# Kernel tuning notes

Measured on AMD Instinct MI355X. Metric: run time of the kernel, lower is better.

Reference implementation:

```python
import jax, jax.numpy as jnp
import numpy as np

B, T, DM, H, DQ, FF, L, OUT = 4, 512, 768, 8, 32, 3072, 6, 80
D_REL = 100   # relative_positional_distance
NEG = 1e8
LN_EPS = 1e-5


def _layer_norm(x, w, b):
    mu = jnp.mean(x, axis=-1, keepdims=True)
    var = jnp.mean((x - mu) ** 2, axis=-1, keepdims=True)
    return (x - mu) * jax.lax.rsqrt(var + LN_EPS) * w + b


def _attention(x, wq, wk, wv, wo, rel):
    # x: (B,T,DM); wq/wk/wv: (H,DM,DQ); wo: (H,DQ,DM); rel: (H, 2*D_REL-1, DQ)
    Tq = x.shape[1]
    q = jnp.einsum('btf,hfa->bhta', x, wq) / (DQ ** 0.5)   # q pre-scaled (as in source)
    k = jnp.einsum('btf,hfa->bhta', x, wk)
    v = jnp.einsum('btf,hfa->bhta', x, wv)
    logits = jnp.einsum('bhqa,bhka->bhqk', q, k)

    # relative positional logits over the 199 learned offsets
    rel_log = jnp.einsum('bhqd,hmd->bhqm', q, rel)          # (B,H,T,2*D_REL-1)
    pad = Tq - D_REL
    if pad > 0:
        # zero-pad to 2T-1 rel positions, then mask out-of-range offsets with -1e8
        rel_log = jnp.pad(rel_log, ((0, 0), (0, 0), (0, 0), (pad, pad)))
        m = jnp.arange(2 * Tq - 1)
        oob = (m < pad) | (m >= 2 * Tq - 1 - pad)
        rel_log = rel_log - NEG * oob.astype(rel_log.dtype)
    else:
        start = D_REL - Tq
        rel_log = rel_log[..., start:start + 2 * Tq - 1]
    # relative -> absolute indexing: pos[..., i, j] = rel_log[..., i, (j - i) + T - 1]
    idx = jnp.arange(Tq)[None, :] - jnp.arange(Tq)[:, None] + (Tq - 1)   # (T,T)
    pos = jnp.take_along_axis(rel_log, idx[None, None], axis=-1)         # (B,H,T,T)

    probs = jax.nn.softmax(logits + pos, axis=-1)
    o = jnp.einsum('bhqk,bhka->bhqa', probs, v)
    return jnp.einsum('bhta,had->btd', o, wo)


def _forward(x, wq, wk, wv, wo, rel, lin1_w, lin1_b, lin2_w, lin2_b,
             ln1_w, ln1_b, ln2_w, ln2_b, w_out, b_out):
    def step(h, p):
        (q, k, v, o, r, l1w, l1b, l2w, l2b, n1w, n1b, n2w, n2b) = p
        a = _attention(h, q, k, v, o, r)
        h = _layer_norm(h + a, n1w, n1b)                  # post-norm, residual
        ff = jnp.maximum(h @ l1w.T + l1b, 0.0) @ l2w.T + l2b
        h = _layer_norm(h + ff, n2w, n2b)
        return h, None
    h, _ = jax.lax.scan(step, x, (wq, wk, wv, wo, rel, lin1_w, lin1_b,
                                  lin2_w, lin2_b, ln1_w, ln1_b, ln2_w, ln2_b))
    return h @ w_out.T + b_out                            # (B,T,OUT)


def setup_inputs() -> dict:
    key = jax.random.key(0)
    ks = jax.random.split(key, 16)
    n = lambda k, shape, scale: (jax.random.normal(k, shape, dtype=jnp.float32) * scale)
    s_qkv = (2.0 / (DM + DQ)) ** 0.5      # xavier_normal_ scale
    s_o = (2.0 / (DQ + DM)) ** 0.5
    return {
        'x':      n(ks[0], (B, T, DM), 1.0),
        'wq':     n(ks[1], (L, H, DM, DQ), s_qkv),
        'wk':     n(ks[2], (L, H, DM, DQ), s_qkv),
        'wv':     n(ks[3], (L, H, DM, DQ), s_qkv),
        'wo':     n(ks[4], (L, H, DQ, DM), s_o),
        'rel':    n(ks[5], (L, H, 2 * D_REL - 1, DQ), DQ ** -0.5),
        'lin1_w': n(ks[6], (L, FF, DM), DM ** -0.5),
        'lin1_b': jnp.zeros((L, FF), jnp.float32),
        'lin2_w': n(ks[7], (L, DM, FF), FF ** -0.5),
        'lin2_b': jnp.zeros((L, DM), jnp.float32),
        'ln1_w':  jnp.ones((L, DM), jnp.float32),
        'ln1_b':  jnp.zeros((L, DM), jnp.float32),
        'ln2_w':  jnp.ones((L, DM), jnp.float32),
        'ln2_b':  jnp.zeros((L, DM), jnp.float32),
        'w_out':  n(ks[8], (OUT, DM), DM ** -0.5),
        'b_out':  jnp.zeros((OUT,), jnp.float32),
    }


def reference(x, wq, wk, wv, wo, rel, lin1_w, lin1_b, lin2_w, lin2_b,
              ln1_w, ln1_b, ln2_w, ln2_b, w_out, b_out):
    return _forward(x, wq, wk, wv, wo, rel, lin1_w, lin1_b, lin2_w, lin2_b,
                    ln1_w, ln1_b, ln2_w, ln2_b, w_out, b_out)
```

## Files before the change

kernel.cpp:

```cpp
#include <hip/hip_runtime.h>

typedef _Float16 f16;
typedef f16 f16x8 __attribute__((ext_vector_type(8)));
typedef f16 f16x4 __attribute__((ext_vector_type(4)));
typedef float f32x4 __attribute__((ext_vector_type(4)));

#define B_ 4
#define T_ 512
#define DM_ 768
#define H_ 8
#define DQ_ 32
#define FF_ 3072
#define L_ 6
#define OUT_ 80
#define M_ (B_*T_)

__device__ __forceinline__ void gload16(const f16* g, f16* l) {
    __builtin_amdgcn_global_load_lds(
        (const __attribute__((address_space(1))) unsigned int*)g,
        (__attribute__((address_space(3))) unsigned int*)l, 16, 0, 0);
}

template<int N> __device__ __forceinline__ void wait_vm() {
    if constexpr (N == 0)      asm volatile("s_waitcnt vmcnt(0)" ::: "memory");
    else if constexpr (N == 3) asm volatile("s_waitcnt vmcnt(3)" ::: "memory");
    else if constexpr (N == 4) asm volatile("s_waitcnt vmcnt(4)" ::: "memory");
    else if constexpr (N == 6) asm volatile("s_waitcnt vmcnt(6)" ::: "memory");
    else                       asm volatile("s_waitcnt vmcnt(0)" ::: "memory");
}


#define PKU_X  98304L
#define PKU_L1 (PKU_X + 884736L)
#define PKU_L2 (PKU_L1 + 884736L)
#define PKB_VEC 7296
#define PKB_LIN 1632
#define PKB_QKV 864
#define PKB_WO  1152
#define PKB_TOTAL (PKB_VEC + PKB_LIN + PKB_QKV + PKB_WO)

__global__ void pack_all_kernel(
    const float* __restrict__ x, const float* __restrict__ wq, const float* __restrict__ wk,
    const float* __restrict__ wv, const float* __restrict__ wo, const float* __restrict__ rel,
    const float* __restrict__ lin1w, const float* __restrict__ lin2w, const float* __restrict__ wout,
    f16* __restrict__ xH, f16* __restrict__ BTqkv, f16* __restrict__ BTwo,
    f16* __restrict__ lin1H, f16* __restrict__ lin2H, f16* __restrict__ woutH, f16* __restrict__ relH)
{
    __shared__ float tile[64 * 65];
    const int bid = blockIdx.x, tid = threadIdx.x;
    if (bid < PKB_VEC) {
        const long u = (long)bid * 256 + tid;
        const float* src; f16* dst; long off;
        if (u < PKU_X)       { src = x;     dst = xH;    off = u; }
        else if (u < PKU_L1) { src = lin1w; dst = lin1H; off = u - PKU_X; }
        else                 { src = lin2w; dst = lin2H; off = u - PKU_L1; }
        const float4 v0 = ((const float4*)src)[off * 4];
        const float4 v1 = ((const float4*)src)[off * 4 + 1];
        const float4 v2 = ((const float4*)src)[off * 4 + 2];
        const float4 v3 = ((const float4*)src)[off * 4 + 3];
        f16x8 o0, o1;
        o0[0] = (f16)v0.x; o0[1] = (f16)v0.y; o0[2] = (f16)v0.z; o0[3] = (f16)v0.w;
        o0[4] = (f16)v1.x; o0[5] = (f16)v1.y; o0[6] = (f16)v1.z; o0[7] = (f16)v1.w;
        o1[0] = (f16)v2.x; o1[1] = (f16)v2.y; o1[2] = (f16)v2.z; o1[3] = (f16)v2.w;
        o1[4] = (f16)v3.x; o1[5] = (f16)v3.y; o1[6] = (f16)v3.z; o1[7] = (f16)v3.w;
        ((f16x8*)dst)[off * 2]     = o0;
        ((f16x8*)dst)[off * 2 + 1] = o1;
    } else if (bid < PKB_VEC + PKB_LIN) {
        const long u = (long)(bid - PKB_VEC) * 256 + tid;
        if (u < 98304) {
            const int k = (int)(u % 768), n = (int)(u / 768);
            woutH[u] = (n < OUT_) ? (f16)wout[n * 768 + k] : (f16)0;
        } else {
            const long v2 = u - 98304;
            const int a = (int)(v2 & 31);
            const long t = v2 >> 5;
            const int d = (int)(t % 208);
            const int lh = (int)(t / 208);
            relH[v2] = (d < 199) ? (f16)rel[((long)lh * 199 + d) * 32 + a] : (f16)0;
        }
    } else if (bid < PKB_VEC + PKB_LIN + PKB_QKV) {
        const int g = bid - (PKB_VEC + PKB_LIN);
        const int kb = g % 12;
        const int grp = g / 12;
        const int hp = grp & 3, sec = (grp >> 2) % 3, l = grp / 12;
        const float* w = (sec == 0) ? wq : (sec == 1 ? wk : wv);
        const float scale = (sec == 0) ? 0.17677669529663687f : 1.f;
#pragma unroll
        for (int hh = 0; hh < 2; ++hh) {
            const float* src = w + (((long)l * 8 + hp * 2 + hh) * 768 + kb * 64) * 32;
#pragma unroll
            for (int p = 0; p < 2; ++p) {
                const int kk = p * 32 + (tid >> 3), a = (tid & 7) * 4;
                const float4 v = *(const float4*)(src + (long)kk * 32 + a);
                float* t = &tile[kk * 65 + hh * 32 + a];
                t[0] = v.x * scale; t[1] = v.y * scale; t[2] = v.z * scale; t[3] = v.w * scale;
            }
        }
        __syncthreads();
        f16* dst = BTqkv + ((long)l * 768 + sec * 256 + hp * 64) * 768 + kb * 64;
#pragma unroll
        for (int p = 0; p < 2; ++p) {
            const int nn = p * 32 + (tid >> 3), k8 = (tid & 7) * 8;
            f16x8 o;
#pragma unroll
            for (int e = 0; e < 8; ++e) o[e] = (f16)tile[(k8 + e) * 65 + nn];
            *(f16x8*)(dst + (long)nn * 768 + k8) = o;
        }
    } else {
        const int g = bid - (PKB_VEC + PKB_LIN + PKB_QKV);
        const int nb = g % 24;
        const int tmp = g / 24;
        const int kb2 = tmp % 8, l = tmp / 8;
        const float* src = wo + ((long)l * 256 + kb2 * 32) * 768 + nb * 32;
        {
            const int r = tid >> 3, c = (tid & 7) * 4;
            const float4 v = *(const float4*)(src + (long)r * 768 + c);
            float* t = &tile[r * 65 + c];
            t[0] = v.x; t[1] = v.y; t[2] = v.z; t[3] = v.w;
        }
        __syncthreads();
        if (tid < 128) {
            const int n = tid >> 2, k8 = (tid & 3) * 8;
            f16x8 o;
#pragma unroll
            for (int e = 0; e < 8; ++e) o[e] = (f16)tile[(k8 + e) * 65 + n];
            f16* dst = BTwo + ((long)l * 768 + nb * 32 + n) * 256 + kb2 * 32 + k8;
            *(f16x8*)dst = o;
        }
    }
}

__device__ __forceinline__ void xcd_tile(int BM, int BN, int& m0, int& n0) {
    const int gx = gridDim.x;
    const int id = blockIdx.y * gx + blockIdx.x;
    const int cpx = (gx * gridDim.y) >> 3;
    const int t = (id & 7) * cpx + (id >> 3);
    m0 = (t / gx) * BM;
    n0 = (t % gx) * BN;
}


template<int BM, int BN>
__global__ __launch_bounds__(256) void gemm7_kernel(
    const f16* __restrict__ A, const f16* __restrict__ Bt,
    const float* __restrict__ bias, const float* __restrict__ res,
    float* __restrict__ outF, f16* __restrict__ outH, f16* __restrict__ vTout,
    int M, int N, int K, int mode, int ldOut, int nMax)
{
    constexpr int IA = BM / 32;
    constexpr int JF = BN / 32;
    constexpr int LA = BM / 32;
    constexpr int LB = BN / 32;
    constexpr int L  = LA + LB;
    __shared__ __align__(16) f16 As[2][BM * 64];
    __shared__ __align__(16) f16 Bs[2][BN * 64];
    const int tid = threadIdx.x;
    const int wave = tid >> 6, lane = tid & 63;
    int m0, n0; xcd_tile(BM, BN, m0, n0);
    const int z = blockIdx.z;
    const int Kl = K / (int)gridDim.z;
    const int kb = z * Kl;
    const int nt = Kl / 64;
    const int wr = wave >> 1, wc = wave & 1;
    const int l15 = lane & 15, l4 = lane >> 4;
    const int lrow = lane >> 3;
    const int lcol = ((lane & 7) ^ (lane >> 3)) * 8;

    const f16* Abase = A  + (long)(m0 + lrow) * K + kb + lcol;
    const f16* Bbase = Bt + (long)(n0 + lrow) * K + kb + lcol;

    f32x4 acc[IA][JF];
#pragma unroll
    for (int i = 0; i < IA; ++i)
#pragma unroll
        for (int j = 0; j < JF; ++j) acc[i][j] = (f32x4){0.f, 0.f, 0.f, 0.f};

    auto stage = [&](int buf, int k0) {
#pragma unroll
        for (int i = 0; i < LA; ++i) {
            const int c = wave + 4 * i;
            gload16(Abase + (long)c * 8 * K + k0, &As[buf][c * 512]);
        }
#pragma unroll
        for (int i = 0; i < LB; ++i) {
            const int c = wave + 4 * i;
            gload16(Bbase + (long)c * 8 * K + k0, &Bs[buf][c * 512]);
        }
    };

    stage(0, 0);
    int cur = 0;
    for (int t = 0; t < nt; ++t) {
        if (t + 1 < nt) { stage(cur ^ 1, (t + 1) * 64); wait_vm<L>(); }
        else            { wait_vm<0>(); }
        __builtin_amdgcn_s_barrier();
#pragma unroll
        for (int s = 0; s < 2; ++s) {
            f16x8 af[IA], bf[JF];
#pragma unroll
            for (int i = 0; i < IA; ++i) {
                const int row = wr * (BM / 2) + i * 16 + l15;
                af[i] = *(const f16x8*)&As[cur][row * 64 + (((s * 4 + l4) ^ (l15 & 7)) * 8)];
            }
#pragma unroll
            for (int j = 0; j < JF; ++j) {
                const int row = wc * (BN / 2) + j * 16 + l15;
                bf[j] = *(const f16x8*)&Bs[cur][row * 64 + (((s * 4 + l4) ^ (l15 & 7)) * 8)];
            }
#pragma unroll
            for (int i = 0; i < IA; ++i)
#pragma unroll
                for (int j = 0; j < JF; ++j)
                    acc[i][j] = __builtin_amdgcn_mfma_f32_16x16x32_f16(af[i], bf[j], acc[i][j], 0, 0, 0);
        }
        __builtin_amdgcn_s_barrier();
        cur ^= 1;
    }

#pragma unroll
    for (int i = 0; i < IA; ++i) {
#pragma unroll
        for (int j = 0; j < JF; ++j) {
            const int col = n0 + wc * (BN / 2) + j * 16 + l15;
            if (mode & 32) {
#pragma unroll
                for (int r = 0; r < 4; ++r) {
                    const int row = m0 + wr * (BM / 2) + i * 16 + l4 * 4 + r;
                    float v = acc[i][j][r];
                    if (col < 512) {
                        outH[(long)row * 512 + col] = (f16)v;
                    } else {
                        const int bb = row >> 9, t = row & 511;
                        vTout[((long)(bb * 256 + (col - 512))) * 512 + t] = (f16)v;
                    }
                }
            } else if (mode & 64) {
                f16* po = outH + (long)z * M * ldOut;
#pragma unroll
                for (int r = 0; r < 4; ++r) {
                    const int row = m0 + wr * (BM / 2) + i * 16 + l4 * 4 + r;
                    po[(long)row * ldOut + col] = (f16)acc[i][j][r];
                }
            } else if (col < nMax) {
                const float bvv = (mode & 1) ? bias[col] : 0.f;
#pragma unroll
                for (int r = 0; r < 4; ++r) {
                    const int row = m0 + wr * (BM / 2) + i * 16 + l4 * 4 + r;
                    float v = acc[i][j][r] + bvv;
                    if (mode & 2) v += res[(long)row * N + col];
                    if (mode & 4) v = fmaxf(v, 0.f);
                    if (mode & 8)  outF[(long)row * ldOut + col] = v;
                    if (mode & 16) outH[(long)row * ldOut + col] = (f16)v;
                }
            }
        }
    }
}


__global__ __launch_bounds__(256) void attn_kernel(
    const f16* __restrict__ qkvH, const f16* __restrict__ vT,
    const f16* __restrict__ relH, int l, f16* __restrict__ o)
{
    __shared__ __align__(16) f16 Ks[272 * 40];
    __shared__ __align__(16) f16 Vt[32 * 296];
    __shared__ __align__(16) f16 Scr[64 * 296];
    const int tid = threadIdx.x;
    const int qb = blockIdx.x, h = blockIdx.y, b = blockIdx.z;
    const int q0 = qb * 64;
    int lo = q0 - 99; lo = (lo > 0) ? (lo & ~7) : 0;
    const int hi = min(512, q0 + 163);
    const int nk = hi - lo;

    for (int idx = tid; idx < 272 * 4; idx += 256) {
        const int r = idx >> 2, c = idx & 3;
        f16x8 v = {};
        if (r < nk)
            v = *(const f16x8*)(qkvH + ((long)(b * 512 + lo + r)) * 512 + 256 + h * 32 + c * 8);
        *(f16x8*)&Ks[r * 40 + c * 8] = v;
    }
    for (int idx = tid; idx < 32 * 36; idx += 256) {
        const int a = idx / 36, k8 = idx % 36;
        f16x8 v = {};
        const int kbase = k8 * 8;
        if (kbase < nk) {
            const f16* src = vT + ((long)(b * 256 + h * 32 + a)) * 512 + lo + kbase;
            if (kbase + 8 <= nk) {
                v = *(const f16x8*)src;
            } else {
#pragma unroll
                for (int e = 0; e < 8; ++e) if (kbase + e < nk) v[e] = src[e];
            }
        }
        *(f16x8*)&Vt[a * 296 + kbase] = v;
    }

    const int wave = tid >> 6, lane = tid & 63;
    const int l15 = lane & 15, l4 = lane >> 4;
    const int qloc = wave * 16;

    const f16x8 qf = *(const f16x8*)(qkvH + ((long)(b * 512 + q0 + qloc + l15)) * 512 + h * 32 + l4 * 8);

    const f16* relh = relH + ((long)(l * 8 + h)) * 208 * 32;
    {
        f32x4 racc[13];
#pragma unroll
        for (int fd = 0; fd < 13; ++fd) {
            const f16x8 bf = *(const f16x8*)(relh + (fd * 16 + l15) * 32 + l4 * 8);
            racc[fd] = __builtin_amdgcn_mfma_f32_16x16x32_f16(qf, bf, (f32x4){0.f,0.f,0.f,0.f}, 0, 0, 0);
        }
#pragma unroll
        for (int fd = 0; fd < 13; ++fd)
#pragma unroll
            for (int r = 0; r < 4; ++r)
                Scr[(qloc + l4 * 4 + r) * 296 + fd * 16 + l15] = (f16)racc[fd][r];
    }
    __syncthreads();

    f32x4 sacc[17];
#pragma unroll
    for (int fk = 0; fk < 17; ++fk) {
        const f16x8 bf = *(const f16x8*)&Ks[(fk * 16 + l15) * 40 + l4 * 8];
        sacc[fk] = __builtin_amdgcn_mfma_f32_16x16x32_f16(qf, bf, (f32x4){0.f,0.f,0.f,0.f}, 0, 0, 0);
    }

    float mx[4] = {-1e30f, -1e30f, -1e30f, -1e30f};
#pragma unroll
    for (int fk = 0; fk < 17; ++fk) {
        const int kk = fk * 16 + l15;
        const int k = lo + kk;
#pragma unroll
        for (int r = 0; r < 4; ++r) {
            const int q = q0 + qloc + l4 * 4 + r;
            const int d = k - q + 99;
            float v = -1e30f;
            if (kk < nk && d >= 0 && d < 199)
                v = sacc[fk][r] + (float)Scr[(qloc + l4 * 4 + r) * 296 + d];
            sacc[fk][r] = v;
            mx[r] = fmaxf(mx[r], v);
        }
    }
#pragma unroll
    for (int r = 0; r < 4; ++r) {
        mx[r] = fmaxf(mx[r], __shfl_xor(mx[r], 1));
        mx[r] = fmaxf(mx[r], __shfl_xor(mx[r], 2));
        mx[r] = fmaxf(mx[r], __shfl_xor(mx[r], 4));
        mx[r] = fmaxf(mx[r], __shfl_xor(mx[r], 8));
    }
    float sum[4] = {0.f, 0.f, 0.f, 0.f};
#pragma unroll
    for (int fk = 0; fk < 17; ++fk) {
        const int kk = fk * 16 + l15;
#pragma unroll
        for (int r = 0; r < 4; ++r) {
            const float p = __expf(sacc[fk][r] - mx[r]);
            sum[r] += p;
            Scr[(qloc + l4 * 4 + r) * 296 + kk] = (f16)p;
        }
    }
#pragma unroll
    for (int r = 0; r < 4; ++r)
        Scr[(qloc + l4 * 4 + r) * 296 + 272 + l15] = (f16)0;
#pragma unroll
    for (int r = 0; r < 4; ++r) {
        sum[r] += __shfl_xor(sum[r], 1);
        sum[r] += __shfl_xor(sum[r], 2);
        sum[r] += __shfl_xor(sum[r], 4);
        sum[r] += __shfl_xor(sum[r], 8);
    }

    f32x4 oacc[2] = {{0.f,0.f,0.f,0.f}, {0.f,0.f,0.f,0.f}};
#pragma unroll
    for (int ks = 0; ks < 9; ++ks) {
        const f16x8 pa = *(const f16x8*)&Scr[(qloc + l15) * 296 + ks * 32 + l4 * 8];
#pragma unroll
        for (int j = 0; j < 2; ++j) {
            const f16x8 vb = *(const f16x8*)&Vt[(j * 16 + l15) * 296 + ks * 32 + l4 * 8];
            oacc[j] = __builtin_amdgcn_mfma_f32_16x16x32_f16(pa, vb, oacc[j], 0, 0, 0);
        }
    }

    f16* ob = o + ((long)(b * 512 + q0 + qloc + l4 * 4)) * 256 + h * 32;
#pragma unroll
    for (int r = 0; r < 4; ++r) {
        const float inv = 1.f / sum[r];
#pragma unroll
        for (int j = 0; j < 2; ++j)
            ob[(long)r * 256 + j * 16 + l15] = (f16)(oacc[j][r] * inv);
    }
}


__global__ __launch_bounds__(256) void ln_kernel(
    const float* __restrict__ src, const float* __restrict__ w, const float* __restrict__ bb,
    float* __restrict__ outF, f16* __restrict__ outH)
{
    __shared__ float red1[4], red2[4];
    const int row = blockIdx.x, tid = threadIdx.x;
    const float* x = src + (long)row * 768;
    float v0 = x[tid], v1 = x[tid + 256], v2 = x[tid + 512];
    float s = v0 + v1 + v2;
#pragma unroll
    for (int off = 32; off > 0; off >>= 1) s += __shfl_xor(s, off);
    if ((tid & 63) == 0) red1[tid >> 6] = s;
    __syncthreads();
    const float mu = (red1[0] + red1[1] + red1[2] + red1[3]) * (1.f / 768.f);
    const float d0 = v0 - mu, d1 = v1 - mu, d2 = v2 - mu;
    float ss = d0 * d0 + d1 * d1 + d2 * d2;
#pragma unroll
    for (int off = 32; off > 0; off >>= 1) ss += __shfl_xor(ss, off);
    if ((tid & 63) == 0) red2[tid >> 6] = ss;
    __syncthreads();
    const float var = (red2[0] + red2[1] + red2[2] + red2[3]) * (1.f / 768.f);
    const float inv = rsqrtf(var + 1e-5f);
    float y0 = d0 * inv * w[tid]       + bb[tid];
    float y1 = d1 * inv * w[tid + 256] + bb[tid + 256];
    float y2 = d2 * inv * w[tid + 512] + bb[tid + 512];
    long base = (long)row * 768;
    outF[base + tid] = y0; outF[base + tid + 256] = y1; outF[base + tid + 512] = y2;
    outH[base + tid] = (f16)y0; outH[base + tid + 256] = (f16)y1; outH[base + tid + 512] = (f16)y2;
}


__global__ __launch_bounds__(256) void ln_sum4_kernel(
    const f16* __restrict__ p,
    const float* __restrict__ bias, const float* __restrict__ res,
    const float* __restrict__ w, const float* __restrict__ bb,
    float* __restrict__ outF, f16* __restrict__ outH)
{
    __shared__ float red1[4], red2[4];
    const int row = blockIdx.x, tid = threadIdx.x;
    const long rb = (long)row * 768;
    float v[3];
#pragma unroll
    for (int i = 0; i < 3; ++i) {
        const int c = tid + i * 256;
        float s = bias[c] + res[rb + c];
#pragma unroll
        for (int zz = 0; zz < 4; ++zz) s += (float)p[((long)zz * M_ + row) * 768 + c];
        v[i] = s;
    }
    float s = v[0] + v[1] + v[2];
#pragma unroll
    for (int off = 32; off > 0; off >>= 1) s += __shfl_xor(s, off);
    if ((tid & 63) == 0) red1[tid >> 6] = s;
    __syncthreads();
    const float mu = (red1[0] + red1[1] + red1[2] + red1[3]) * (1.f / 768.f);
    const float d0 = v[0] - mu, d1 = v[1] - mu, d2 = v[2] - mu;
    float ss = d0 * d0 + d1 * d1 + d2 * d2;
#pragma unroll
    for (int off = 32; off > 0; off >>= 1) ss += __shfl_xor(ss, off);
    if ((tid & 63) == 0) red2[tid >> 6] = ss;
    __syncthreads();
    const float var = (red2[0] + red2[1] + red2[2] + red2[3]) * (1.f / 768.f);
    const float inv = rsqrtf(var + 1e-5f);
    float y0 = d0 * inv * w[tid]       + bb[tid];
    float y1 = d1 * inv * w[tid + 256] + bb[tid + 256];
    float y2 = d2 * inv * w[tid + 512] + bb[tid + 512];
    outF[rb + tid] = y0; outF[rb + tid + 256] = y1; outF[rb + tid + 512] = y2;
    outH[rb + tid] = (f16)y0; outH[rb + tid + 256] = (f16)y1; outH[rb + tid + 512] = (f16)y2;
}


extern "C" void kernel_launch(void* const* d_in, const int* in_sizes, int n_in,
                              void* d_out, int out_size, void* d_ws, size_t ws_size,
                              hipStream_t stream) {
    const float* x     = (const float*)d_in[0];
    const float* wq    = (const float*)d_in[1];
    const float* wk    = (const float*)d_in[2];
    const float* wv    = (const float*)d_in[3];
    const float* wo    = (const float*)d_in[4];
    const float* rel   = (const float*)d_in[5];
    const float* lin1w = (const float*)d_in[6];
    const float* lin1b = (const float*)d_in[7];
    const float* lin2w = (const float*)d_in[8];
    const float* lin2b = (const float*)d_in[9];
    const float* ln1w  = (const float*)d_in[10];
    const float* ln1b  = (const float*)d_in[11];
    const float* ln2w  = (const float*)d_in[12];
    const float* ln2b  = (const float*)d_in[13];
    const float* wout  = (const float*)d_in[14];
    const float* bout  = (const float*)d_in[15];

    char* base = (char*)d_ws;
    size_t off = 0;
    auto alloc = [&](size_t bytes) {
        void* p = base + off;
        off = (off + bytes + 255) & ~(size_t)255;
        return p;
    };
    f16*   xH    = (f16*)  alloc((size_t)M_ * 768 * 2);
    f16*   BTqkv = (f16*)  alloc((size_t)L_ * 768 * 768 * 2);
    f16*   BTwo  = (f16*)  alloc((size_t)L_ * 768 * 256 * 2);
    f16*   lin1H = (f16*)  alloc((size_t)L_ * 3072 * 768 * 2);
    f16*   lin2H = (f16*)  alloc((size_t)L_ * 768 * 3072 * 2);
    f16*   woutH = (f16*)  alloc((size_t)128 * 768 * 2);
    f16*   relH  = (f16*)  alloc((size_t)L_ * 8 * 208 * 32 * 2);
    f16*   qkvH  = (f16*)  alloc((size_t)M_ * 512 * 2);
    f16*   vTbuf = (f16*)  alloc((size_t)B_ * 256 * 512 * 2);
    float* scrF  = (float*)alloc((size_t)M_ * 768 * 4);
    f16*   partH = (f16*)  alloc((size_t)4 * M_ * 768 * 2);
    f16*   oH    = (f16*)  alloc((size_t)M_ * 256 * 2);
    float* ln1F  = (float*)alloc((size_t)M_ * 768 * 4);
    f16*   ln1H  = (f16*)  alloc((size_t)M_ * 768 * 2);
    f16*   ffH   = (f16*)  alloc((size_t)M_ * 3072 * 2);
    float* hF    = (float*)alloc((size_t)M_ * 768 * 4);
    f16*   hH    = (f16*)  alloc((size_t)M_ * 768 * 2);
    (void)ws_size; (void)in_sizes; (void)n_in; (void)out_size;

    pack_all_kernel<<<PKB_TOTAL, 256, 0, stream>>>(
        x, wq, wk, wv, wo, rel, lin1w, lin2w, wout,
        xH, BTqkv, BTwo, lin1H, lin2H, woutH, relH);

    for (int l = 0; l < L_; ++l) {
        const f16*   aIn   = (l == 0) ? xH : hH;
        const float* resIn = (l == 0) ? x  : hF;
        gemm7_kernel<32, 64><<<dim3(12, 64, 1), 256, 0, stream>>>(
            aIn, BTqkv + (size_t)l * 768 * 768, nullptr, nullptr, nullptr, qkvH, vTbuf,
            M_, 768, 768, 32, 512, 768);
        attn_kernel<<<dim3(8, 8, 4), 256, 0, stream>>>(qkvH, vTbuf, relH, l, oH);
        gemm7_kernel<32, 64><<<dim3(12, 64, 1), 256, 0, stream>>>(
            oH, BTwo + (size_t)l * 768 * 256, nullptr, resIn, scrF, nullptr, nullptr,
            M_, 768, 256, 2 | 8, 768, 768);
        ln_kernel<<<M_, 256, 0, stream>>>(scrF, ln1w + l * 768, ln1b + l * 768, ln1F, ln1H);
        gemm7_kernel<128, 64><<<dim3(48, 16, 1), 256, 0, stream>>>(
            ln1H, lin1H + (size_t)l * 3072 * 768, lin1b + l * 3072, nullptr, nullptr, ffH, nullptr,
            M_, 3072, 768, 1 | 4 | 16, 3072, 3072);
        gemm7_kernel<128, 64><<<dim3(12, 16, 4), 256, 0, stream>>>(
            ffH, lin2H + (size_t)l * 768 * 3072, nullptr, nullptr, nullptr, partH, nullptr,
            M_, 768, 3072, 64, 768, 768);
        ln_sum4_kernel<<<M_, 256, 0, stream>>>(partH, lin2b + l * 768, ln1F,
                                               ln2w + l * 768, ln2b + l * 768, hF, hH);
    }
    gemm7_kernel<32, 64><<<dim3(2, 64, 1), 256, 0, stream>>>(
        hH, woutH, bout, nullptr, (float*)d_out, nullptr, nullptr,
        M_, 80, 768, 1 | 8, 80, 80);
}
```

Before: 501.7 us.

## Add intra-block split-K GEMM for small-N projections and nontemporal pack stores

Adds a gemm8 kernel for the QKV, output-projection and final-head GEMMs. It uses a 128-wide K stage per iteration, and the four waves split into two K halves that are reduced through shared memory before the epilogue. Each wave handles a 32x32 output slice instead of the full tile height, which gives more MFMA work per barrier and fewer K iterations on these short-K GEMMs. Weight and activation packing stores become nontemporal, and gemm7 drops its now-unused QKV scatter mode. The trade-offs are a larger shared-memory footprint and an extra reduction step.

```diff
diff --git a/kernel.cpp b/kernel.cpp
--- a/kernel.cpp
+++ b/kernel.cpp
@@ -63,8 +63,8 @@
         o0[4] = (f16)v1.x; o0[5] = (f16)v1.y; o0[6] = (f16)v1.z; o0[7] = (f16)v1.w;
         o1[0] = (f16)v2.x; o1[1] = (f16)v2.y; o1[2] = (f16)v2.z; o1[3] = (f16)v2.w;
         o1[4] = (f16)v3.x; o1[5] = (f16)v3.y; o1[6] = (f16)v3.z; o1[7] = (f16)v3.w;
-        ((f16x8*)dst)[off * 2]     = o0;
-        ((f16x8*)dst)[off * 2 + 1] = o1;
+        __builtin_nontemporal_store(o0, (f16x8*)dst + off * 2);
+        __builtin_nontemporal_store(o1, (f16x8*)dst + off * 2 + 1);
     } else if (bid < PKB_VEC + PKB_LIN) {
         const long u = (long)(bid - PKB_VEC) * 256 + tid;
         if (u < 98304) {
@@ -104,7 +104,7 @@
             f16x8 o;
 #pragma unroll
             for (int e = 0; e < 8; ++e) o[e] = (f16)tile[(k8 + e) * 65 + nn];
-            *(f16x8*)(dst + (long)nn * 768 + k8) = o;
+            __builtin_nontemporal_store(o, (f16x8*)(dst + (long)nn * 768 + k8));
         }
     } else {
         const int g = bid - (PKB_VEC + PKB_LIN + PKB_QKV);
@@ -125,7 +125,7 @@
 #pragma unroll
             for (int e = 0; e < 8; ++e) o[e] = (f16)tile[(k8 + e) * 65 + n];
             f16* dst = BTwo + ((long)l * 768 + nb * 32 + n) * 256 + kb2 * 32 + k8;
-            *(f16x8*)dst = o;
+            __builtin_nontemporal_store(o, (f16x8*)dst);
         }
     }
 }
@@ -222,10 +222,127 @@
 #pragma unroll
         for (int j = 0; j < JF; ++j) {
             const int col = n0 + wc * (BN / 2) + j * 16 + l15;
-            if (mode & 32) {
+            if (mode & 64) {
+                f16* po = outH + (long)z * M * ldOut;
 #pragma unroll
                 for (int r = 0; r < 4; ++r) {
                     const int row = m0 + wr * (BM / 2) + i * 16 + l4 * 4 + r;
+                    po[(long)row * ldOut + col] = (f16)acc[i][j][r];
+                }
+            } else if (col < nMax) {
+                const float bvv = (mode & 1) ? bias[col] : 0.f;
+#pragma unroll
+                for (int r = 0; r < 4; ++r) {
+                    const int row = m0 + wr * (BM / 2) + i * 16 + l4 * 4 + r;
+                    float v = acc[i][j][r] + bvv;
+                    if (mode & 2) v += res[(long)row * N + col];
+                    if (mode & 4) v = fmaxf(v, 0.f);
+                    if (mode & 8)  outF[(long)row * ldOut + col] = v;
+                    if (mode & 16) outH[(long)row * ldOut + col] = (f16)v;
+                }
+            }
+        }
+    }
+}
+
+
+__global__ __launch_bounds__(256) void gemm8_kernel(
+    const f16* __restrict__ A, const f16* __restrict__ Bt,
+    const float* __restrict__ bias, const float* __restrict__ res,
+    float* __restrict__ outF, f16* __restrict__ outH, f16* __restrict__ vTout,
+    int M, int N, int K, int mode, int ldOut, int nMax)
+{
+    __shared__ __align__(16) f16 As[2][32 * 128];
+    __shared__ __align__(16) f16 Bs[2][64 * 128];
+    const int tid = threadIdx.x;
+    const int wave = tid >> 6, lane = tid & 63;
+    int m0, n0; xcd_tile(32, 64, m0, n0);
+    const int nt = K / 128;
+    const int kw = wave >> 1, wc = wave & 1;
+    const int l15 = lane & 15, l4 = lane >> 4;
+    const int srow = lane >> 4;
+
+    f32x4 acc[2][2];
+#pragma unroll
+    for (int i = 0; i < 2; ++i)
+#pragma unroll
+        for (int j = 0; j < 2; ++j) acc[i][j] = (f32x4){0.f, 0.f, 0.f, 0.f};
+
+    auto stage = [&](int buf, int k0) {
+#pragma unroll
+        for (int i = 0; i < 2; ++i) {
+            const int c = wave + 4 * i;
+            const int gsw = (lane & 15) ^ ((c * 4 + srow) & 7);
+            gload16(A + (long)(m0 + c * 4 + srow) * K + k0 + gsw * 8, &As[buf][c * 512]);
+        }
+#pragma unroll
+        for (int i = 0; i < 4; ++i) {
+            const int c = wave + 4 * i;
+            const int gsw = (lane & 15) ^ ((c * 4 + srow) & 7);
+            gload16(Bt + (long)(n0 + c * 4 + srow) * K + k0 + gsw * 8, &Bs[buf][c * 512]);
+        }
+    };
+
+    stage(0, 0);
+    int cur = 0;
+    for (int t = 0; t < nt; ++t) {
+        if (t + 1 < nt) { stage(cur ^ 1, (t + 1) * 128); wait_vm<6>(); }
+        else            { wait_vm<0>(); }
+        __builtin_amdgcn_s_barrier();
+#pragma unroll
+        for (int s = 0; s < 2; ++s) {
+            f16x8 af[2], bf[2];
+#pragma unroll
+            for (int i = 0; i < 2; ++i) {
+                const int row = i * 16 + l15;
+                af[i] = *(const f16x8*)&As[cur][row * 128 + (((kw * 8 + s * 4 + l4) ^ (row & 7)) * 8)];
+            }
+#pragma unroll
+            for (int j = 0; j < 2; ++j) {
+                const int row = wc * 32 + j * 16 + l15;
+                bf[j] = *(const f16x8*)&Bs[cur][row * 128 + (((kw * 8 + s * 4 + l4) ^ (row & 7)) * 8)];
+            }
+#pragma unroll
+            for (int i = 0; i < 2; ++i)
+#pragma unroll
+                for (int j = 0; j < 2; ++j)
+                    acc[i][j] = __builtin_amdgcn_mfma_f32_16x16x32_f16(af[i], bf[j], acc[i][j], 0, 0, 0);
+        }
+        __builtin_amdgcn_s_barrier();
+        cur ^= 1;
+    }
+
+    float* red = (float*)&As[0][0];
+    if (kw == 1) {
+        const int base = (wc * 64 + lane) * 17;
+#pragma unroll
+        for (int i = 0; i < 2; ++i)
+#pragma unroll
+            for (int j = 0; j < 2; ++j)
+#pragma unroll
+                for (int r = 0; r < 4; ++r)
+                    red[base + i * 8 + j * 4 + r] = acc[i][j][r];
+    }
+    __syncthreads();
+    if (kw != 0) return;
+    const int base = (wc * 64 + lane) * 17;
+#pragma unroll
+    for (int i = 0; i < 2; ++i)
+#pragma unroll
+        for (int j = 0; j < 2; ++j)
+#pragma unroll
+            for (int r = 0; r < 4; ++r)
+                acc[i][j][r] += red[base + i * 8 + j * 4 + r];
+
+#pragma unroll
+    for (int i = 0; i < 2; ++i) {
+#pragma unroll
+        for (int j = 0; j < 2; ++j) {
+            const int col = n0 + wc * 32 + j * 16 + l15;
+            if (mode & 32) {
+#pragma unroll
+                for (int r = 0; r < 4; ++r) {
+                    const int row = m0 + i * 16 + l4 * 4 + r;
                     float v = acc[i][j][r];
                     if (col < 512) {
                         outH[(long)row * 512 + col] = (f16)v;
@@ -234,23 +351,14 @@
                         vTout[((long)(bb * 256 + (col - 512))) * 512 + t] = (f16)v;
                     }
                 }
-            } else if (mode & 64) {
-                f16* po = outH + (long)z * M * ldOut;
-#pragma unroll
-                for (int r = 0; r < 4; ++r) {
-                    const int row = m0 + wr * (BM / 2) + i * 16 + l4 * 4 + r;
-                    po[(long)row * ldOut + col] = (f16)acc[i][j][r];
-                }
             } else if (col < nMax) {
                 const float bvv = (mode & 1) ? bias[col] : 0.f;
 #pragma unroll
                 for (int r = 0; r < 4; ++r) {
-                    const int row = m0 + wr * (BM / 2) + i * 16 + l4 * 4 + r;
+                    const int row = m0 + i * 16 + l4 * 4 + r;
                     float v = acc[i][j][r] + bvv;
                     if (mode & 2) v += res[(long)row * N + col];
-                    if (mode & 4) v = fmaxf(v, 0.f);
-                    if (mode & 8)  outF[(long)row * ldOut + col] = v;
-                    if (mode & 16) outH[(long)row * ldOut + col] = (f16)v;
+                    if (mode & 8) outF[(long)row * ldOut + col] = v;
                 }
             }
         }
@@ -515,11 +623,11 @@
     for (int l = 0; l < L_; ++l) {
         const f16*   aIn   = (l == 0) ? xH : hH;
         const float* resIn = (l == 0) ? x  : hF;
-        gemm7_kernel<32, 64><<<dim3(12, 64, 1), 256, 0, stream>>>(
+        gemm8_kernel<<<dim3(12, 64, 1), 256, 0, stream>>>(
             aIn, BTqkv + (size_t)l * 768 * 768, nullptr, nullptr, nullptr, qkvH, vTbuf,
             M_, 768, 768, 32, 512, 768);
         attn_kernel<<<dim3(8, 8, 4), 256, 0, stream>>>(qkvH, vTbuf, relH, l, oH);
-        gemm7_kernel<32, 64><<<dim3(12, 64, 1), 256, 0, stream>>>(
+        gemm8_kernel<<<dim3(12, 64, 1), 256, 0, stream>>>(
             oH, BTwo + (size_t)l * 768 * 256, nullptr, resIn, scrF, nullptr, nullptr,
             M_, 768, 256, 2 | 8, 768, 768);
         ln_kernel<<<M_, 256, 0, stream>>>(scrF, ln1w + l * 768, ln1b + l * 768, ln1F, ln1H);
@@ -532,7 +640,7 @@
         ln_sum4_kernel<<<M_, 256, 0, stream>>>(partH, lin2b + l * 768, ln1F,
                                                ln2w + l * 768, ln2b + l * 768, hF, hH);
     }
-    gemm7_kernel<32, 64><<<dim3(2, 64, 1), 256, 0, stream>>>(
+    gemm8_kernel<<<dim3(2, 64, 1), 256, 0, stream>>>(
         hH, woutH, bout, nullptr, (float*)d_out, nullptr, nullptr,
         M_, 80, 768, 1 | 8, 80, 80);
 }
```

Result: slower. 551.2 us (+9.9%).
